# Kernel tuning notes

Hardware: AMD Instinct MI355X
Metric: run time of the kernel (lower is better)

Reference implementation:

```python
import jax, jax.numpy as jnp
import numpy as np

N = 50000       # nodes
E_RAND = 800000 # random edges (avg degree ~16)
K = 64          # edges touching `node`; setup_inputs guarantees exactly K
F = 64          # num_node_features
C = 64          # conv_channels


def setup_inputs() -> dict:
    key = jax.random.key(0)
    ks = jax.random.split(key, 6)
    x = jax.random.normal(ks[0], (N, F), dtype=jnp.float32)
    # random edges avoiding node 0 so exactly the K prepended edges touch node 0
    src = jax.random.randint(ks[1], (E_RAND,), 1, N, dtype=jnp.int64)
    dst = jax.random.randint(ks[2], (E_RAND,), 1, N, dtype=jnp.int64)
    ksrc = jnp.zeros((K,), dtype=jnp.int64)
    kdst = jnp.arange(1, K + 1, dtype=jnp.int64)
    edge_index = jnp.stack([jnp.concatenate([ksrc, src]),
                            jnp.concatenate([kdst, dst])])  # [2, K+E_RAND]
    W1 = jax.random.normal(ks[3], (F, C), jnp.float32) / np.float32(np.sqrt(F))
    b1 = jnp.zeros((C,), jnp.float32)
    W2 = jax.random.normal(ks[4], (C, C), jnp.float32) / np.float32(np.sqrt(C))
    b2 = jnp.zeros((C,), jnp.float32)
    Wr = jax.random.normal(ks[5], (C, 1), jnp.float32) / np.float32(np.sqrt(C))
    br = jnp.zeros((1,), jnp.float32)
    return {"x": x, "edge_index": edge_index, "node": 0,
            "W1": W1, "b1": b1, "W2": W2, "b2": b2, "Wr": Wr, "br": br}


def gcn_conv(x, src, dst, W, b):
    """PyG GCNConv with self-loops already appended to (src, dst).
    out[v] = sum_{(u,v)} deg(u)^-1/2 * deg(v)^-1/2 * (x @ W)[u] + b
    """
    n = x.shape[0]
    xw = x @ W                                              # [N, C]
    deg = jnp.zeros((n,), xw.dtype).at[dst].add(1.0)        # in-degree incl. self-loop
    dinv = jnp.where(deg > 0, jax.lax.rsqrt(deg), 0.0)
    norm = dinv[src] * dinv[dst]                            # [E]
    out = jax.ops.segment_sum(xw[src] * norm[:, None], dst, num_segments=n)
    return out + b


def reference(x, edge_index, node, W1, b1, W2, b2, Wr, br):
    n = x.shape[0]
    loop = jnp.arange(n, dtype=edge_index.dtype)
    src = jnp.concatenate([edge_index[0], loop])  # add self loops (GCNConv default)
    dst = jnp.concatenate([edge_index[1], loop])
    h = jax.nn.relu(gcn_conv(x, src, dst, W1, b1))
    h = jax.nn.relu(gcn_conv(h, src, dst, W2, b2))
    # edges incident to `node` (setup guarantees exactly K such edges)
    s0, d0 = edge_index[0], edge_index[1]
    mask = (s0 == node) | (d0 == node)
    idx = jnp.nonzero(mask, size=K)[0]
    s, d = s0[idx], d0[idx]
    targets = jnp.where(s == node, d, s)  # self-loop (s==d==node) -> node
    score = h[targets] @ Wr + br          # [K, 1]
    score = jax.nn.softmax(score, axis=0)
    return score[:, 0], targets
```

## Files before the change

kernel.cpp:

```cpp
#include <hip/hip_runtime.h>
#include <math.h>

#define KK 64
#define CAP 64
#define NF 4160
#define HSZ 8192
#define BMW 1568

__global__ __launch_bounds__(256) void k_find(const int* __restrict__ ei, int E,
                                              const int* __restrict__ nodep,
                                              int4* __restrict__ zbase, int zcount4,
                                              int* __restrict__ tcount,
                                              int* __restrict__ tpairs,
                                              float* __restrict__ h1s) {
    int idx = blockIdx.x * 256 + threadIdx.x;
    if (idx < zcount4) zbase[idx] = make_int4(0, 0, 0, 0);
    if (idx < 64) h1s[(size_t)NF * 64 + idx] = 0.f;
    int node = nodep[0];
    int n4 = E >> 2;
    if (idx < n4) {
        int4 ss = ((const int4*)ei)[idx];
        int4 dd = ((const int4*)(ei + E))[idx];
        int s[4] = {ss.x, ss.y, ss.z, ss.w};
        int d[4] = {dd.x, dd.y, dd.z, dd.w};
#pragma unroll
        for (int k = 0; k < 4; k++) {
            if (s[k] == node || d[k] == node) {
                int q = atomicAdd(tcount, 1);
                if (q < KK) { int e = idx * 4 + k; tpairs[2 * q] = e; tpairs[2 * q + 1] = (s[k] == node) ? d[k] : s[k]; }
            }
        }
    }
    if (idx == 0) {
        for (int e = n4 * 4; e < E; e++) {
            int s = ei[e], d = ei[E + e];
            if (s == node || d == node) {
                int q = atomicAdd(tcount, 1);
                if (q < KK) { tpairs[2 * q] = e; tpairs[2 * q + 1] = (s == node) ? d : s; }
            }
        }
    }
}

__global__ __launch_bounds__(256) void k_collect_t(const int* __restrict__ ei, int E,
                                                   const int* __restrict__ tpairs,
                                                   int* __restrict__ cnt,
                                                   int* __restrict__ tcnt2,
                                                   int* __restrict__ tslots,
                                                   int* __restrict__ tsorted_g,
                                                   int* __restrict__ towner_g) {
    __shared__ unsigned int bmask[BMW];
    __shared__ int tnode[KK];
    __shared__ int eidx[KK], tgt[KK], srt[KK];
    int tid = threadIdx.x;
    for (int i = tid; i < BMW; i += 256) bmask[i] = 0u;
    if (tid < KK) { eidx[tid] = tpairs[2 * tid]; tgt[tid] = tpairs[2 * tid + 1]; }
    __syncthreads();
    if (tid < KK) {
        int rank = 0;
        for (int j = 0; j < KK; j++) rank += (eidx[j] < eidx[tid]) ? 1 : 0;
        srt[rank] = tgt[tid];
    }
    __syncthreads();
    if (tid < KK) {
        int mynode = srt[tid];
        int owner = tid;
        for (int j = 0; j < tid; j++) if (srt[j] == mynode) { owner = j; break; }
        tnode[tid] = (owner == tid) ? mynode : -1;
        if (owner == tid) atomicOr(&bmask[mynode >> 5], 1u << (mynode & 31));
        if (blockIdx.x == 0) { tsorted_g[tid] = mynode; towner_g[tid] = owner; }
    }
    __syncthreads();
    int n4 = E >> 2;
    for (int idx = blockIdx.x * 256 + tid; idx < n4; idx += gridDim.x * 256) {
        int4 ss = ((const int4*)ei)[idx];
        int4 dd = ((const int4*)(ei + E))[idx];
        int s[4] = {ss.x, ss.y, ss.z, ss.w};
        int d[4] = {dd.x, dd.y, dd.z, dd.w};
        atomicAdd(&cnt[d[0]], 1);
        atomicAdd(&cnt[d[1]], 1);
#pragma unroll
        for (int k = 0; k < 4; k++) {
            if ((bmask[d[k] >> 5] >> (d[k] & 31)) & 1u) {
                int f = 0;
                for (int j = 0; j < KK; j++) if (tnode[j] == d[k]) { f = j + 1; break; }
                if (f) { int p = atomicAdd(&tcnt2[f - 1], 1); if (p < CAP) tslots[(f - 1) * CAP + p] = s[k]; }
            }
        }
    }
    if (blockIdx.x == 0 && tid == 0) {
        for (int e = n4 * 4; e < E; e++) {
            int d = ei[E + e];
            atomicAdd(&cnt[d], 1);
            if ((bmask[d >> 5] >> (d & 31)) & 1u) {
                int f = 0;
                for (int j = 0; j < KK; j++) if (tnode[j] == d) { f = j + 1; break; }
                if (f) { int p = atomicAdd(&tcnt2[f - 1], 1); if (p < CAP) tslots[(f - 1) * CAP + p] = ei[e]; }
            }
        }
    }
}

__device__ __forceinline__ int fnode_of(int i, const int* tsorted, const int* towner,
                                        const int* tcnt2, const int* tslots) {
    int tp = i / 65, j = i % 65;
    if (j == 0) return tsorted[tp];
    int own = towner[tp];
    int c = tcnt2[own]; if (c > CAP) c = CAP;
    return (j - 1 < c) ? tslots[own * CAP + (j - 1)] : -1;
}

__global__ __launch_bounds__(256) void k_collect_f(const int* __restrict__ ei, int E,
                                                   const int* __restrict__ tsorted,
                                                   const int* __restrict__ towner,
                                                   const int* __restrict__ tcnt2,
                                                   const int* __restrict__ tslots,
                                                   int* __restrict__ cnt,
                                                   int* __restrict__ fcnt,
                                                   int* __restrict__ fslots,
                                                   int* __restrict__ fnode_g,
                                                   int* __restrict__ fidx_g,
                                                   unsigned char* __restrict__ fown_g) {
    __shared__ unsigned int hmap[HSZ];
    int tid = threadIdx.x;
    for (int i = tid; i < HSZ; i += 256) hmap[i] = 0xFFFFFFFFu;
    __syncthreads();
    for (int i = tid; i < NF; i += 256) {
        int u = fnode_of(i, tsorted, towner, tcnt2, tslots);
        if (u >= 0) {
            unsigned int packed = ((unsigned)u << 16) | (unsigned)i;
            unsigned int slot = (((unsigned)u * 2654435761u) >> 13) & (HSZ - 1);
            while (true) {
                unsigned int cur = hmap[slot];
                if (cur == 0xFFFFFFFFu) {
                    unsigned int old = atomicCAS(&hmap[slot], 0xFFFFFFFFu, packed);
                    if (old == 0xFFFFFFFFu) break;
                    cur = old;
                }
                if ((cur >> 16) == (unsigned)u) {
                    if ((cur & 0xFFFFu) <= (unsigned)i) break;
                    if (atomicCAS(&hmap[slot], cur, packed) == cur) break;
                } else {
                    slot = (slot + 1) & (HSZ - 1);
                }
            }
        }
    }
    __syncthreads();
    if (blockIdx.x == 0) {
        for (int i = tid; i < NF; i += 256) {
            int u = fnode_of(i, tsorted, towner, tcnt2, tslots);
            int row = NF, isown = 0;
            if (u >= 0) {
                unsigned int slot = (((unsigned)u * 2654435761u) >> 13) & (HSZ - 1);
                while (true) {
                    unsigned int cur = hmap[slot];
                    if ((cur >> 16) == (unsigned)u) { row = (int)(cur & 0xFFFFu); break; }
                    slot = (slot + 1) & (HSZ - 1);
                }
                isown = (row == i);
            }
            fnode_g[i] = u; fidx_g[i] = row; fown_g[i] = (unsigned char)isown;
        }
    }
    int n4 = E >> 2;
    for (int idx = blockIdx.x * 256 + tid; idx < n4; idx += gridDim.x * 256) {
        int4 ss = ((const int4*)ei)[idx];
        int4 dd = ((const int4*)(ei + E))[idx];
        int s[4] = {ss.x, ss.y, ss.z, ss.w};
        int d[4] = {dd.x, dd.y, dd.z, dd.w};
        atomicAdd(&cnt[d[2]], 1);
        atomicAdd(&cnt[d[3]], 1);
#pragma unroll
        for (int k = 0; k < 4; k++) {
            unsigned int key = (unsigned)d[k];
            unsigned int slot = ((key * 2654435761u) >> 13) & (HSZ - 1);
            int row = -1;
            while (true) {
                unsigned int cur = hmap[slot];
                if (cur == 0xFFFFFFFFu) break;
                if ((cur >> 16) == key) { row = (int)(cur & 0xFFFFu); break; }
                slot = (slot + 1) & (HSZ - 1);
            }
            if (row >= 0) { int p = atomicAdd(&fcnt[row], 1); if (p < CAP) fslots[(size_t)row * CAP + p] = s[k]; }
        }
    }
    if (blockIdx.x == 0 && tid == 0) {
        for (int e = n4 * 4; e < E; e++) {
            unsigned int key = (unsigned)ei[E + e];
            unsigned int slot = ((key * 2654435761u) >> 13) & (HSZ - 1);
            int row = -1;
            while (true) {
                unsigned int cur = hmap[slot];
                if (cur == 0xFFFFFFFFu) break;
                if ((cur >> 16) == key) { row = (int)(cur & 0xFFFFu); break; }
                slot = (slot + 1) & (HSZ - 1);
            }
            if (row >= 0) { int p = atomicAdd(&fcnt[row], 1); if (p < CAP) fslots[(size_t)row * CAP + p] = ei[e]; }
        }
    }
}

__global__ __launch_bounds__(256) void k_layer1(const float* __restrict__ x,
                                                const int* __restrict__ fnode,
                                                const unsigned char* __restrict__ fown,
                                                const int* __restrict__ cnt,
                                                const int* __restrict__ fcnt,
                                                const int* __restrict__ fslots,
                                                const float* __restrict__ W1,
                                                const float* __restrict__ b1,
                                                float* __restrict__ h1s) {
    __shared__ __align__(16) float W1s[64 * 64];
    int tid = threadIdx.x;
    for (int i = tid; i < 1024; i += 256) ((float4*)W1s)[i] = ((const float4*)W1)[i];
    __syncthreads();
    int i = blockIdx.x * 4 + (tid >> 6);
    int lane = tid & 63;
    if (i >= NF) return;
    if (!fown[i]) return;
    int u = fnode[i];
    float du = rsqrtf((float)(cnt[u] + 1));
    float acc = du * x[(size_t)u * 64 + lane];
    int c = fcnt[i]; if (c > CAP) c = CAP;
    const int* sl = fslots + (size_t)i * CAP;
    int k = 0;
    for (; k + 4 <= c; k += 4) {
        int u0 = sl[k], u1 = sl[k + 1], u2 = sl[k + 2], u3 = sl[k + 3];
        float f0 = rsqrtf((float)(cnt[u0] + 1));
        float f1 = rsqrtf((float)(cnt[u1] + 1));
        float f2 = rsqrtf((float)(cnt[u2] + 1));
        float f3 = rsqrtf((float)(cnt[u3] + 1));
        acc += f0 * x[(size_t)u0 * 64 + lane] + f1 * x[(size_t)u1 * 64 + lane]
             + f2 * x[(size_t)u2 * 64 + lane] + f3 * x[(size_t)u3 * 64 + lane];
    }
    for (; k < c; k++) {
        int uu = sl[k];
        acc += rsqrtf((float)(cnt[uu] + 1)) * x[(size_t)uu * 64 + lane];
    }
    float z = du * acc;
    float h = 0.f;
#pragma unroll
    for (int f = 0; f < 64; f++) h += __shfl(z, f) * W1s[f * 64 + lane];
    h = fmaxf(h + b1[lane], 0.f);
    h1s[(size_t)i * 64 + lane] = du * h;
}

__global__ __launch_bounds__(64) void k_score2(const float* __restrict__ h1s,
                                               const int* __restrict__ fidx,
                                               const int* __restrict__ tsorted,
                                               const int* __restrict__ cnt,
                                               const float* __restrict__ W2,
                                               const float* __restrict__ b2,
                                               const float* __restrict__ Wr,
                                               float* __restrict__ sc) {
    int tp = blockIdx.x;
    int lane = threadIdx.x;
    int t = tsorted[tp];
    float dt = rsqrtf((float)(cnt[t] + 1));
    const int* fx = fidx + tp * 65;
    float z = 0.f;
#pragma unroll
    for (int j = 0; j < 65; j++) {
        int idx = fx[j];
        z += h1s[(size_t)idx * 64 + lane];
    }
    z *= dt;
    float acc = 0.f;
#pragma unroll
    for (int f = 0; f < 64; f++) acc += __shfl(z, f) * W2[f * 64 + lane];
    float h2 = fmaxf(acc + b2[lane], 0.f);
    float p = h2 * Wr[lane];
#pragma unroll
    for (int off = 32; off >= 1; off >>= 1) p += __shfl_xor(p, off);
    if (lane == 0) sc[tp] = p;
}

__global__ void k_softmax(const float* __restrict__ sc, const int* __restrict__ tsorted,
                          float* __restrict__ out) {
    int t = threadIdx.x;
    float s = sc[t];
    float m = s;
#pragma unroll
    for (int off = 32; off >= 1; off >>= 1) m = fmaxf(m, __shfl_xor(m, off));
    float e = __expf(s - m);
    float ss = e;
#pragma unroll
    for (int off = 32; off >= 1; off >>= 1) ss += __shfl_xor(ss, off);
    out[t] = e / ss;
    out[KK + t] = (float)tsorted[t];
}

extern "C" void kernel_launch(void* const* d_in, const int* in_sizes, int n_in,
                              void* d_out, int out_size, void* d_ws, size_t ws_size,
                              hipStream_t stream) {
    const float* x  = (const float*)d_in[0];
    const int*   ei = (const int*)d_in[1];
    const int*   nodep = (const int*)d_in[2];
    const float* W1 = (const float*)d_in[3];
    const float* b1 = (const float*)d_in[4];
    const float* W2 = (const float*)d_in[5];
    const float* b2 = (const float*)d_in[6];
    const float* Wr = (const float*)d_in[7];
    const float* br = (const float*)d_in[8];
    float* out = (float*)d_out;
    (void)br;

    int N = in_sizes[0] / 64;
    int E = in_sizes[1] / 2;

    char* w = (char*)d_ws;
    int* cnt    = (int*)w; w += (size_t)N * 4;
    int* fcnt   = (int*)w; w += (size_t)NF * 4;
    int* tcnt2  = (int*)w; w += KK * 4;
    int zcount4 = (N + NF + KK) / 4;
    int* tcount = (int*)w; w += 16;
    int* tpairs  = (int*)w; w += 2 * KK * 4;
    int* tsorted = (int*)w; w += KK * 4;
    int* towner  = (int*)w; w += KK * 4;
    int* tslots  = (int*)w; w += (size_t)KK * CAP * 4;
    int* fnode   = (int*)w; w += (size_t)NF * 4;
    int* fidx    = (int*)w; w += (size_t)NF * 4;
    unsigned char* fown = (unsigned char*)w; w += (size_t)NF;
    w = (char*)(((size_t)w + 15) & ~(size_t)15);
    int* fslots  = (int*)w; w += (size_t)NF * CAP * 4;
    float* h1s   = (float*)w; w += (size_t)(NF + 1) * 64 * 4;
    float* sc    = (float*)w; w += KK * 4;

    hipMemsetAsync(tcount, 0, 16, stream);

    int n4 = E >> 2;
    int ebl = (n4 + 255) / 256;
    k_find<<<ebl, 256, 0, stream>>>(ei, E, nodep, (int4*)cnt, zcount4, tcount, tpairs, h1s);
    k_collect_t<<<512, 256, 0, stream>>>(ei, E, tpairs, cnt, tcnt2, tslots, tsorted, towner);
    k_collect_f<<<512, 256, 0, stream>>>(ei, E, tsorted, towner, tcnt2, tslots,
                                         cnt, fcnt, fslots, fnode, fidx, fown);
    k_layer1<<<(NF + 3) / 4, 256, 0, stream>>>(x, fnode, fown, cnt, fcnt, fslots, W1, b1, h1s);
    k_score2<<<KK, 64, 0, stream>>>(h1s, fidx, tsorted, cnt, W2, b2, Wr, sc);
    k_softmax<<<1, 64, 0, stream>>>(sc, tsorted, out);
}
```

Before: 166.6 us.

## Replace per-block shared hash map with global direct-mapped frontier row table

Each of the 512 blocks used to rebuild a shared-memory hash table of the frontier nodes before scanning edges. A new single-block kernel now builds a direct-indexed global array (node to row+1) once. The edge-scan kernel becomes a one-shot grid that does a single global lookup per edge instead of hash probing. This removes the 512-fold redundant table construction, at the cost of an extra launch, a larger zeroed workspace, and uncached random global reads into a 200KB table.

```diff
diff --git a/kernel.cpp b/kernel.cpp
--- a/kernel.cpp
+++ b/kernel.cpp
@@ -4,7 +4,6 @@
 #define KK 64
 #define CAP 64
 #define NF 4160
-#define HSZ 8192
 #define BMW 1568
 
 __global__ __launch_bounds__(256) void k_find(const int* __restrict__ ei, int E,
@@ -110,93 +109,62 @@
     return (j - 1 < c) ? tslots[own * CAP + (j - 1)] : -1;
 }
 
+__global__ __launch_bounds__(1024) void k_fbuild(const int* __restrict__ tsorted,
+                                                 const int* __restrict__ towner,
+                                                 const int* __restrict__ tcnt2,
+                                                 const int* __restrict__ tslots,
+                                                 int* __restrict__ fnode,
+                                                 int* __restrict__ fmapRow,
+                                                 int* __restrict__ fidx,
+                                                 unsigned char* __restrict__ fown) {
+    int tid = threadIdx.x;
+    for (int i = tid; i < NF; i += 1024)
+        fnode[i] = fnode_of(i, tsorted, towner, tcnt2, tslots);
+    __syncthreads();
+    for (int i = tid; i < NF; i += 1024) {
+        int u = fnode[i];
+        if (u >= 0) atomicCAS(&fmapRow[u], 0, i + 1);
+    }
+    __syncthreads();
+    for (int i = tid; i < NF; i += 1024) {
+        int u = fnode[i];
+        if (u >= 0) {
+            int row = fmapRow[u];
+            fidx[i] = row - 1;
+            fown[i] = (unsigned char)(row == i + 1);
+        } else {
+            fidx[i] = NF;
+            fown[i] = 0;
+        }
+    }
+}
+
 __global__ __launch_bounds__(256) void k_collect_f(const int* __restrict__ ei, int E,
-                                                   const int* __restrict__ tsorted,
-                                                   const int* __restrict__ towner,
-                                                   const int* __restrict__ tcnt2,
-                                                   const int* __restrict__ tslots,
+                                                   const int* __restrict__ fmapRow,
                                                    int* __restrict__ cnt,
                                                    int* __restrict__ fcnt,
-                                                   int* __restrict__ fslots,
-                                                   int* __restrict__ fnode_g,
-                                                   int* __restrict__ fidx_g,
-                                                   unsigned char* __restrict__ fown_g) {
-    __shared__ unsigned int hmap[HSZ];
-    int tid = threadIdx.x;
-    for (int i = tid; i < HSZ; i += 256) hmap[i] = 0xFFFFFFFFu;
-    __syncthreads();
-    for (int i = tid; i < NF; i += 256) {
-        int u = fnode_of(i, tsorted, towner, tcnt2, tslots);
-        if (u >= 0) {
-            unsigned int packed = ((unsigned)u << 16) | (unsigned)i;
-            unsigned int slot = (((unsigned)u * 2654435761u) >> 13) & (HSZ - 1);
-            while (true) {
-                unsigned int cur = hmap[slot];
-                if (cur == 0xFFFFFFFFu) {
-                    unsigned int old = atomicCAS(&hmap[slot], 0xFFFFFFFFu, packed);
-                    if (old == 0xFFFFFFFFu) break;
-                    cur = old;
-                }
-                if ((cur >> 16) == (unsigned)u) {
-                    if ((cur & 0xFFFFu) <= (unsigned)i) break;
-                    if (atomicCAS(&hmap[slot], cur, packed) == cur) break;
-                } else {
-                    slot = (slot + 1) & (HSZ - 1);
-                }
-            }
-        }
-    }
-    __syncthreads();
-    if (blockIdx.x == 0) {
-        for (int i = tid; i < NF; i += 256) {
-            int u = fnode_of(i, tsorted, towner, tcnt2, tslots);
-            int row = NF, isown = 0;
-            if (u >= 0) {
-                unsigned int slot = (((unsigned)u * 2654435761u) >> 13) & (HSZ - 1);
-                while (true) {
-                    unsigned int cur = hmap[slot];
-                    if ((cur >> 16) == (unsigned)u) { row = (int)(cur & 0xFFFFu); break; }
-                    slot = (slot + 1) & (HSZ - 1);
-                }
-                isown = (row == i);
-            }
-            fnode_g[i] = u; fidx_g[i] = row; fown_g[i] = (unsigned char)isown;
-        }
-    }
+                                                   int* __restrict__ fslots) {
+    int idx = blockIdx.x * 256 + threadIdx.x;
     int n4 = E >> 2;
-    for (int idx = blockIdx.x * 256 + tid; idx < n4; idx += gridDim.x * 256) {
+    if (idx < n4) {
         int4 ss = ((const int4*)ei)[idx];
         int4 dd = ((const int4*)(ei + E))[idx];
         int s[4] = {ss.x, ss.y, ss.z, ss.w};
         int d[4] = {dd.x, dd.y, dd.z, dd.w};
         atomicAdd(&cnt[d[2]], 1);
         atomicAdd(&cnt[d[3]], 1);
-#pragma unroll
-        for (int k = 0; k < 4; k++) {
-            unsigned int key = (unsigned)d[k];
-            unsigned int slot = ((key * 2654435761u) >> 13) & (HSZ - 1);
-            int row = -1;
-            while (true) {
-                unsigned int cur = hmap[slot];
-                if (cur == 0xFFFFFFFFu) break;
-                if ((cur >> 16) == key) { row = (int)(cur & 0xFFFFu); break; }
-                slot = (slot + 1) & (HSZ - 1);
-            }
-            if (row >= 0) { int p = atomicAdd(&fcnt[row], 1); if (p < CAP) fslots[(size_t)row * CAP + p] = s[k]; }
-        }
-    }
-    if (blockIdx.x == 0 && tid == 0) {
+        int r0 = fmapRow[d[0]], r1 = fmapRow[d[1]], r2 = fmapRow[d[2]], r3 = fmapRow[d[3]];
+        if (r0) { int p = atomicAdd(&fcnt[r0 - 1], 1); if (p < CAP) fslots[(size_t)(r0 - 1) * CAP + p] = s[0]; }
+        if (r1) { int p = atomicAdd(&fcnt[r1 - 1], 1); if (p < CAP) fslots[(size_t)(r1 - 1) * CAP + p] = s[1]; }
+        if (r2) { int p = atomicAdd(&fcnt[r2 - 1], 1); if (p < CAP) fslots[(size_t)(r2 - 1) * CAP + p] = s[2]; }
+        if (r3) { int p = atomicAdd(&fcnt[r3 - 1], 1); if (p < CAP) fslots[(size_t)(r3 - 1) * CAP + p] = s[3]; }
+    }
+    if (idx == 0) {
         for (int e = n4 * 4; e < E; e++) {
-            unsigned int key = (unsigned)ei[E + e];
-            unsigned int slot = ((key * 2654435761u) >> 13) & (HSZ - 1);
-            int row = -1;
-            while (true) {
-                unsigned int cur = hmap[slot];
-                if (cur == 0xFFFFFFFFu) break;
-                if ((cur >> 16) == key) { row = (int)(cur & 0xFFFFu); break; }
-                slot = (slot + 1) & (HSZ - 1);
-            }
-            if (row >= 0) { int p = atomicAdd(&fcnt[row], 1); if (p < CAP) fslots[(size_t)row * CAP + p] = ei[e]; }
+            int d = ei[E + e];
+            atomicAdd(&cnt[d], 1);
+            int r = fmapRow[d];
+            if (r) { int p = atomicAdd(&fcnt[r - 1], 1); if (p < CAP) fslots[(size_t)(r - 1) * CAP + p] = ei[e]; }
         }
     }
 }
@@ -309,10 +277,11 @@
     int E = in_sizes[1] / 2;
 
     char* w = (char*)d_ws;
-    int* cnt    = (int*)w; w += (size_t)N * 4;
-    int* fcnt   = (int*)w; w += (size_t)NF * 4;
-    int* tcnt2  = (int*)w; w += KK * 4;
-    int zcount4 = (N + NF + KK) / 4;
+    int* cnt     = (int*)w; w += (size_t)N * 4;
+    int* fmapRow = (int*)w; w += (size_t)N * 4;
+    int* fcnt    = (int*)w; w += (size_t)NF * 4;
+    int* tcnt2   = (int*)w; w += KK * 4;
+    int zcount4 = (2 * N + NF + KK) / 4;
     int* tcount = (int*)w; w += 16;
     int* tpairs  = (int*)w; w += 2 * KK * 4;
     int* tsorted = (int*)w; w += KK * 4;
@@ -332,8 +301,8 @@
     int ebl = (n4 + 255) / 256;
     k_find<<<ebl, 256, 0, stream>>>(ei, E, nodep, (int4*)cnt, zcount4, tcount, tpairs, h1s);
     k_collect_t<<<512, 256, 0, stream>>>(ei, E, tpairs, cnt, tcnt2, tslots, tsorted, towner);
-    k_collect_f<<<512, 256, 0, stream>>>(ei, E, tsorted, towner, tcnt2, tslots,
-                                         cnt, fcnt, fslots, fnode, fidx, fown);
+    k_fbuild<<<1, 1024, 0, stream>>>(tsorted, towner, tcnt2, tslots, fnode, fmapRow, fidx, fown);
+    k_collect_f<<<ebl, 256, 0, stream>>>(ei, E, fmapRow, cnt, fcnt, fslots);
     k_layer1<<<(NF + 3) / 4, 256, 0, stream>>>(x, fnode, fown, cnt, fcnt, fslots, W1, b1, h1s);
     k_score2<<<KK, 64, 0, stream>>>(h1s, fidx, tsorted, cnt, W2, b2, Wr, sc);
     k_softmax<<<1, 64, 0, stream>>>(sc, tsorted, out);
```

Measured after the change: 152.7 us. 1.09x faster.
